# Kernel tuning notes

Measured on AMD Instinct MI355X. Metric: run time of the kernel, lower is better.

Reference implementation:

```python
import jax, jax.numpy as jnp
import numpy as np


def setup_inputs() -> dict:
    key = jax.random.key(0)
    kq, kk = jax.random.split(key)
    B, T, H, D = 2, 512, 8, 64
    q = jax.random.normal(kq, (B, T, H, D), dtype=jnp.float32)
    k = jax.random.normal(kk, (B, T, H, D), dtype=jnp.float32)
    return {"q": q, "k": k}


def reference(q, k):
    # q, k: [B, T, H, D]; output attn: [B, Tq, Tk, H]
    # attn[b,s,t,h] = -sum_d |q[b,s,h,d] - k[b,t,h,d]| / sqrt(D)
    D = q.shape[-1]
    scale = 1.0 / jnp.sqrt(jnp.float32(D))
    H = q.shape[2]
    # Loop over the small fixed head count (<=8) to avoid a [B,T,T,H,D] intermediate;
    # per head we materialize only [B,Tq,Tk,D].
    heads = []
    for h in range(H):
        qh = q[:, :, h, :]  # [B, Tq, D]
        kh = k[:, :, h, :]  # [B, Tk, D]
        diff = jnp.abs(qh[:, :, None, :] - kh[:, None, :, :])  # [B, Tq, Tk, D]
        heads.append(-jnp.sum(diff, axis=-1) * scale)  # [B, Tq, Tk]
    return jnp.stack(heads, axis=-1)  # [B, Tq, Tk, H]
```

## Files before the change

### kernel.cpp

```cpp
#include <hip/hip_runtime.h>


#define TDIM 512
#define HDIM 8
#define DDIM 64
#define TILE 64
#define PAD  76

__global__ __launch_bounds__(256) void l1attn_kernel(
    const float* __restrict__ q, const float* __restrict__ k,
    float* __restrict__ out)
{
    __shared__ float qs[TILE * PAD];
    __shared__ float ks[TILE * PAD];

    const int t   = threadIdx.x;
    const int jt  = blockIdx.x * TILE;
    const int it  = blockIdx.y * TILE;
    const int bh  = blockIdx.z;
    const int b   = bh >> 3;
    const int h   = bh & 7;

    const float* qb = q + (((size_t)(b * TDIM + it)) * HDIM + h) * DDIM;
    const float* kb = k + (((size_t)(b * TDIM + jt)) * HDIM + h) * DDIM;

    const int lane16 = t & 15;
    const int grp    = t >> 4;

    #pragma unroll
    for (int c = 0; c < 4; ++c) {
        int row = c * 16 + grp;
        float4 vq = *(const float4*)(qb + (size_t)row * (HDIM * DDIM) + lane16 * 4);
        float4 vk = *(const float4*)(kb + (size_t)row * (HDIM * DDIM) + lane16 * 4);
        *(float4*)&qs[row * PAD + lane16 * 4] = vq;
        *(float4*)&ks[row * PAD + lane16 * 4] = vk;
    }
    __syncthreads();

    const int ty = grp;
    const int tx = lane16;

    float acc[4][4];
    #pragma unroll
    for (int r = 0; r < 4; ++r)
        #pragma unroll
        for (int s = 0; s < 4; ++s) acc[r][s] = 0.f;

    #pragma unroll 4
    for (int d = 0; d < DDIM; d += 4) {
        float4 qv[4], kv[4];
        #pragma unroll
        for (int r = 0; r < 4; ++r) qv[r] = *(float4*)&qs[(ty * 4 + r) * PAD + d];
        #pragma unroll
        for (int s = 0; s < 4; ++s) kv[s] = *(float4*)&ks[(tx * 4 + s) * PAD + d];
        #pragma unroll
        for (int r = 0; r < 4; ++r)
            #pragma unroll
            for (int s = 0; s < 4; ++s) {
                acc[r][s] += fabsf(qv[r].x - kv[s].x);
                acc[r][s] += fabsf(qv[r].y - kv[s].y);
                acc[r][s] += fabsf(qv[r].z - kv[s].z);
                acc[r][s] += fabsf(qv[r].w - kv[s].w);
            }
    }

    #pragma unroll
    for (int r = 0; r < 4; ++r) {
        size_t i = it + ty * 4 + r;
        size_t base = ((size_t)(b * TDIM) + i) * TDIM;
        #pragma unroll
        for (int s = 0; s < 4; ++s) {
            size_t j = jt + tx * 4 + s;
            out[(base + j) * HDIM + h] = acc[r][s] * -0.125f;
        }
    }
}

extern "C" void kernel_launch(void* const* d_in, const int* in_sizes, int n_in,
                              void* d_out, int out_size, void* d_ws, size_t ws_size,
                              hipStream_t stream) {
    const float* q = (const float*)d_in[0];
    const float* k = (const float*)d_in[1];
    float* out = (float*)d_out;
    const int B = in_sizes[0] / (TDIM * HDIM * DDIM);
    dim3 grid(TDIM / TILE, TDIM / TILE, B * HDIM);
    l1attn_kernel<<<grid, 256, 0, stream>>>(q, k, out);
}
```

Before: 88.42 us.

## Process all heads per block so output writes cover contiguous head groups

```diff
diff --git a/kernel.cpp b/kernel.cpp
--- a/kernel.cpp
+++ b/kernel.cpp
@@ -4,75 +4,85 @@
 #define TDIM 512
 #define HDIM 8
 #define DDIM 64
-#define TILE 64
-#define PAD  76
+#define ITILE 32
+#define JTILE 32
+#define ROWF 256
+#define PADS 260
 
-__global__ __launch_bounds__(256) void l1attn_kernel(
+__global__ __launch_bounds__(256, 2) void l1attn_kernel(
     const float* __restrict__ q, const float* __restrict__ k,
     float* __restrict__ out)
 {
-    __shared__ float qs[TILE * PAD];
-    __shared__ float ks[TILE * PAD];
+    __shared__ float qs[ITILE * PADS];
+    __shared__ float ks[JTILE * PADS];
 
-    const int t   = threadIdx.x;
-    const int jt  = blockIdx.x * TILE;
-    const int it  = blockIdx.y * TILE;
-    const int bh  = blockIdx.z;
-    const int b   = bh >> 3;
-    const int h   = bh & 7;
+    const int t    = threadIdx.x;
+    const int jt   = blockIdx.x * JTILE;
+    const int it   = blockIdx.y * ITILE;
+    const int b    = blockIdx.z;
 
-    const float* qb = q + (((size_t)(b * TDIM + it)) * HDIM + h) * DDIM;
-    const float* kb = k + (((size_t)(b * TDIM + jt)) * HDIM + h) * DDIM;
-
-    const int lane16 = t & 15;
-    const int grp    = t >> 4;
+    const int w    = t >> 6;
+    const int lane = t & 63;
+    const int tx   = lane & 7;
+    const int ty   = lane >> 3;
 
     #pragma unroll
-    for (int c = 0; c < 4; ++c) {
-        int row = c * 16 + grp;
-        float4 vq = *(const float4*)(qb + (size_t)row * (HDIM * DDIM) + lane16 * 4);
-        float4 vk = *(const float4*)(kb + (size_t)row * (HDIM * DDIM) + lane16 * 4);
-        *(float4*)&qs[row * PAD + lane16 * 4] = vq;
-        *(float4*)&ks[row * PAD + lane16 * 4] = vk;
-    }
-    __syncthreads();
+    for (int p = 0; p < 2; ++p) {
+        #pragma unroll
+        for (int c = 0; c < 8; ++c) {
+            int chunk = c * 256 + t;
+            int row   = chunk >> 6;
+            int col4  = chunk & 63;
+            float4 vq = *(const float4*)(q + ((size_t)(b * TDIM + it + row)) * (HDIM * DDIM)
+                                           + p * ROWF + col4 * 4);
+            float4 vk = *(const float4*)(k + ((size_t)(b * TDIM + jt + row)) * (HDIM * DDIM)
+                                           + p * ROWF + col4 * 4);
+            *(float4*)&qs[row * PADS + col4 * 4] = vq;
+            *(float4*)&ks[row * PADS + col4 * 4] = vk;
+        }
+        __syncthreads();
 
-    const int ty = grp;
-    const int tx = lane16;
+        const float* qbase = &qs[w * DDIM];
+        const float* kbase = &ks[w * DDIM];
 
-    float acc[4][4];
-    #pragma unroll
-    for (int r = 0; r < 4; ++r)
-        #pragma unroll
-        for (int s = 0; s < 4; ++s) acc[r][s] = 0.f;
-
-    #pragma unroll 4
-    for (int d = 0; d < DDIM; d += 4) {
-        float4 qv[4], kv[4];
-        #pragma unroll
-        for (int r = 0; r < 4; ++r) qv[r] = *(float4*)&qs[(ty * 4 + r) * PAD + d];
-        #pragma unroll
-        for (int s = 0; s < 4; ++s) kv[s] = *(float4*)&ks[(tx * 4 + s) * PAD + d];
+        float acc[4][4];
         #pragma unroll
         for (int r = 0; r < 4; ++r)
             #pragma unroll
+            for (int s = 0; s < 4; ++s) acc[r][s] = 0.f;
+
+        #pragma unroll 4
+        for (int d = 0; d < DDIM; d += 4) {
+            float4 qv[4], kv[4];
+            #pragma unroll
+            for (int r = 0; r < 4; ++r)
+                qv[r] = *(const float4*)&qbase[(ty + 8 * r) * PADS + d];
+            #pragma unroll
+            for (int s = 0; s < 4; ++s)
+                kv[s] = *(const float4*)&kbase[(tx + 8 * s) * PADS + d];
+            #pragma unroll
+            for (int r = 0; r < 4; ++r)
+                #pragma unroll
+                for (int s = 0; s < 4; ++s) {
+                    acc[r][s] += fabsf(qv[r].x - kv[s].x);
+                    acc[r][s] += fabsf(qv[r].y - kv[s].y);
+                    acc[r][s] += fabsf(qv[r].z - kv[s].z);
+                    acc[r][s] += fabsf(qv[r].w - kv[s].w);
+                }
+        }
+
+        const int h = p * 4 + w;
+        #pragma unroll
+        for (int r = 0; r < 4; ++r) {
+            size_t i    = (size_t)(it + ty + 8 * r);
+            size_t base = ((size_t)(b * TDIM) + i) * TDIM;
+            #pragma unroll
             for (int s = 0; s < 4; ++s) {
-                acc[r][s] += fabsf(qv[r].x - kv[s].x);
-                acc[r][s] += fabsf(qv[r].y - kv[s].y);
-                acc[r][s] += fabsf(qv[r].z - kv[s].z);
-                acc[r][s] += fabsf(qv[r].w - kv[s].w);
+                size_t j = (size_t)(jt + tx + 8 * s);
+                out[(base + j) * HDIM + h] = acc[r][s] * -0.125f;
             }
-    }
-
-    #pragma unroll
-    for (int r = 0; r < 4; ++r) {
-        size_t i = it + ty * 4 + r;
-        size_t base = ((size_t)(b * TDIM) + i) * TDIM;
-        #pragma unroll
-        for (int s = 0; s < 4; ++s) {
-            size_t j = jt + tx * 4 + s;
-            out[(base + j) * HDIM + h] = acc[r][s] * -0.125f;
         }
+        __syncthreads();
     }
 }
 
@@ -83,6 +93,6 @@
     const float* k = (const float*)d_in[1];
     float* out = (float*)d_out;
     const int B = in_sizes[0] / (TDIM * HDIM * DDIM);
-    dim3 grid(TDIM / TILE, TDIM / TILE, B * HDIM);
+    dim3 grid(TDIM / JTILE, TDIM / ITILE, B);
     l1attn_kernel<<<grid, 256, 0, stream>>>(q, k, out);
 }
```

Measured after the change: 84.76 us. -4.1%, faster.

## Hold K rows in registers, broadcast Q rows, one wave per head

Applied to the files above, without the earlier changes.

```diff
diff --git a/kernel.cpp b/kernel.cpp
--- a/kernel.cpp
+++ b/kernel.cpp
@@ -4,75 +4,43 @@
 #define TDIM 512
 #define HDIM 8
 #define DDIM 64
-#define TILE 64
-#define PAD  76
+#define JBLK 64
+#define IBLK 16
 
-__global__ __launch_bounds__(256) void l1attn_kernel(
+__global__ __launch_bounds__(512, 4) void l1attn_kernel(
     const float* __restrict__ q, const float* __restrict__ k,
     float* __restrict__ out)
 {
-    __shared__ float qs[TILE * PAD];
-    __shared__ float ks[TILE * PAD];
+    const int t    = threadIdx.x;
+    const int lane = t & 63;
+    const int h    = __builtin_amdgcn_readfirstlane(t >> 6);
+    const int j0   = blockIdx.x * JBLK;
+    const int i0   = blockIdx.y * IBLK;
+    const int b    = blockIdx.z;
 
-    const int t   = threadIdx.x;
-    const int jt  = blockIdx.x * TILE;
-    const int it  = blockIdx.y * TILE;
-    const int bh  = blockIdx.z;
-    const int b   = bh >> 3;
-    const int h   = bh & 7;
+    const float* krow = k + (((size_t)(b * TDIM + j0 + lane)) * HDIM + h) * DDIM;
+    float4 kr[16];
+    #pragma unroll
+    for (int c = 0; c < 16; ++c)
+        kr[c] = *(const float4*)(krow + 4 * c);
 
-    const float* qb = q + (((size_t)(b * TDIM + it)) * HDIM + h) * DDIM;
-    const float* kb = k + (((size_t)(b * TDIM + jt)) * HDIM + h) * DDIM;
+    #pragma unroll 2
+    for (int ii = 0; ii < IBLK; ++ii) {
+        const int i = i0 + ii;
+        const float* qrow = q + (((size_t)(b * TDIM + i)) * HDIM + h) * DDIM;
 
-    const int lane16 = t & 15;
-    const int grp    = t >> 4;
+        float a0 = 0.f, a1 = 0.f, a2 = 0.f, a3 = 0.f;
+        #pragma unroll
+        for (int c = 0; c < 16; ++c) {
+            float4 qv = *(const float4*)(qrow + 4 * c);
+            a0 += fabsf(qv.x - kr[c].x);
+            a1 += fabsf(qv.y - kr[c].y);
+            a2 += fabsf(qv.z - kr[c].z);
+            a3 += fabsf(qv.w - kr[c].w);
+        }
+        float acc = (a0 + a1) + (a2 + a3);
 
-    #pragma unroll
-    for (int c = 0; c < 4; ++c) {
-        int row = c * 16 + grp;
-        float4 vq = *(const float4*)(qb + (size_t)row * (HDIM * DDIM) + lane16 * 4);
-        float4 vk = *(const float4*)(kb + (size_t)row * (HDIM * DDIM) + lane16 * 4);
-        *(float4*)&qs[row * PAD + lane16 * 4] = vq;
-        *(float4*)&ks[row * PAD + lane16 * 4] = vk;
-    }
-    __syncthreads();
-
-    const int ty = grp;
-    const int tx = lane16;
-
-    float acc[4][4];
-    #pragma unroll
-    for (int r = 0; r < 4; ++r)
-        #pragma unroll
-        for (int s = 0; s < 4; ++s) acc[r][s] = 0.f;
-
-    #pragma unroll 4
-    for (int d = 0; d < DDIM; d += 4) {
-        float4 qv[4], kv[4];
-        #pragma unroll
-        for (int r = 0; r < 4; ++r) qv[r] = *(float4*)&qs[(ty * 4 + r) * PAD + d];
-        #pragma unroll
-        for (int s = 0; s < 4; ++s) kv[s] = *(float4*)&ks[(tx * 4 + s) * PAD + d];
-        #pragma unroll
-        for (int r = 0; r < 4; ++r)
-            #pragma unroll
-            for (int s = 0; s < 4; ++s) {
-                acc[r][s] += fabsf(qv[r].x - kv[s].x);
-                acc[r][s] += fabsf(qv[r].y - kv[s].y);
-                acc[r][s] += fabsf(qv[r].z - kv[s].z);
-                acc[r][s] += fabsf(qv[r].w - kv[s].w);
-            }
-    }
-
-    #pragma unroll
-    for (int r = 0; r < 4; ++r) {
-        size_t i = it + ty * 4 + r;
-        size_t base = ((size_t)(b * TDIM) + i) * TDIM;
-        #pragma unroll
-        for (int s = 0; s < 4; ++s) {
-            size_t j = jt + tx * 4 + s;
-            out[(base + j) * HDIM + h] = acc[r][s] * -0.125f;
-        }
+        out[((size_t)(b * TDIM + i) * TDIM + (j0 + lane)) * HDIM + h] = acc * -0.125f;
     }
 }
 
@@ -83,6 +51,6 @@
     const float* k = (const float*)d_in[1];
     float* out = (float*)d_out;
     const int B = in_sizes[0] / (TDIM * HDIM * DDIM);
-    dim3 grid(TDIM / TILE, TDIM / TILE, B * HDIM);
-    l1attn_kernel<<<grid, 256, 0, stream>>>(q, k, out);
+    dim3 grid(TDIM / JBLK, TDIM / IBLK, B);
+    l1attn_kernel<<<grid, 512, 0, stream>>>(q, k, out);
 }
```

Result: slower. 161.3 us (+82.4%).
